# Optimization experiments

Hardware: AMD Instinct MI355X
Metric: run time of the kernel (lower is better)

## Reference

```python
import jax, jax.numpy as jnp
import numpy as np

NUM_EMBEDDINGS = 8192
EMBEDDING_DIM = 128


def setup_inputs() -> dict:
    key = jax.random.key(0)
    k1, k2 = jax.random.split(key)
    inputs = jax.random.normal(k1, (8, 32, 32, EMBEDDING_DIM), dtype=jnp.float32)
    embedding_weight = jax.random.normal(k2, (NUM_EMBEDDINGS, EMBEDDING_DIM), dtype=jnp.float32)
    return {"inputs": inputs, "embedding_weight": embedding_weight}


def reference(inputs, embedding_weight):
    # inputs: [B, H, W, C] channels-last; embedding_weight: [K, C]
    input_shape = inputs.shape
    flat_input = inputs.reshape(-1, EMBEDDING_DIM)  # [N, C]

    distances = (
        jnp.sum(flat_input ** 2, axis=1, keepdims=True)
        + jnp.sum(embedding_weight ** 2, axis=1)
        - 2.0 * flat_input @ embedding_weight.T
    )
    encoding_indices = jnp.argmin(distances, axis=1)  # [N]

    # one-hot encodings (returned by the original module)
    encodings = jax.nn.one_hot(encoding_indices, NUM_EMBEDDINGS, dtype=jnp.float32)  # [N, K]

    # quantized via direct gather (same math as one_hot @ weight, no big matmul)
    quantized = embedding_weight[encoding_indices].reshape(input_shape)  # [B,H,W,C]

    # straight-through estimator
    quantized = inputs + jax.lax.stop_gradient(quantized - inputs)

    quantized_nchw = jnp.transpose(quantized, (0, 3, 1, 2))  # [B,C,H,W]
    return quantized_nchw, encodings
```

## Files before the change

### kernel.cpp

```cpp
#include <hip/hip_runtime.h>

typedef _Float16 f16x4 __attribute__((ext_vector_type(4)));
typedef _Float16 f16x8 __attribute__((ext_vector_type(8)));
typedef float    f32x16 __attribute__((ext_vector_type(16)));
typedef float    f32x4v __attribute__((ext_vector_type(4)));

#define HN_OFF   0u
#define BEST_OFF 32768u
#define ERH_OFF  98304u
#define ERL_OFF  (98304u + 2097152u)
#define XRH_OFF  (98304u + 2u * 2097152u)
#define XRL_OFF  (98304u + 3u * 2097152u)

#define OUT_Q    0
#define OUT_ENC  1048576


__device__ __forceinline__ void gll16(const void* g, void* l) {
    __builtin_amdgcn_global_load_lds(
        (const __attribute__((address_space(1))) unsigned int*)g,
        (__attribute__((address_space(3))) unsigned int*)l, 16, 0, 0);
}

__global__ __launch_bounds__(256) void k1_convert(const float* __restrict__ x,
                                                  const float* __restrict__ e,
                                                  char* __restrict__ wsb) {
    int bx = blockIdx.x, tid = threadIdx.x;
    bool is_e = bx < 1024;
    const float* src = is_e ? e : x;
    int sec = is_e ? bx : bx - 1024;
    size_t off = (size_t)sec * 1024 + tid * 4;
    float4 v = *(const float4*)(src + off);

    f16x4 hi, lo;
    hi[0] = (_Float16)v.x; hi[1] = (_Float16)v.y;
    hi[2] = (_Float16)v.z; hi[3] = (_Float16)v.w;
    lo[0] = (_Float16)((v.x - (float)hi[0]) * 2048.0f);
    lo[1] = (_Float16)((v.y - (float)hi[1]) * 2048.0f);
    lo[2] = (_Float16)((v.z - (float)hi[2]) * 2048.0f);
    lo[3] = (_Float16)((v.w - (float)hi[3]) * 2048.0f);

    if (is_e) {
        int code = (int)(off >> 7);
        int c = (tid & 31) * 4;
        int tile = code >> 6, w = code & 63;
        int slot = (c >> 3) ^ (w & 15);
        size_t dst = (size_t)tile * 8192 + w * 128 + slot * 8 + (c & 7);
        *(f16x4*)((_Float16*)(wsb + ERH_OFF) + dst) = hi;
        *(f16x4*)((_Float16*)(wsb + ERL_OFF) + dst) = lo;

        float s = v.x * v.x + v.y * v.y + v.z * v.z + v.w * v.w;
        for (int o = 16; o > 0; o >>= 1) s += __shfl_down(s, o, 32);
        if ((tid & 31) == 0)
            ((float*)(wsb + HN_OFF))[code] = 0.5f * s;
    } else {
        _Float16* ph = (_Float16*)(wsb + XRH_OFF);
        _Float16* pl = (_Float16*)(wsb + XRL_OFF);
        *(f16x4*)(ph + off) = hi;
        *(f16x4*)(pl + off) = lo;
        if (sec < 32)
            ((unsigned long long*)(wsb + BEST_OFF))[sec * 256 + tid] = 0ull;
    }
}

__global__ __launch_bounds__(256, 2) void k2_mfma(char* __restrict__ wsb,
                                                  float* __restrict__ out) {
    __shared__ _Float16 lds_e[2][2][8192];
    __shared__ float    lds_hn[1024];

    const _Float16* xrh = (const _Float16*)(wsb + XRH_OFF);
    const _Float16* xrl = (const _Float16*)(wsb + XRL_OFF);
    const float* hn = (const float*)(wsb + HN_OFF);
    unsigned long long* bestg = (unsigned long long*)(wsb + BEST_OFF);

    int tid = threadIdx.x;
    int lane = tid & 63, wave = tid >> 6;
    int col = lane & 31, half = lane >> 5;
    int m = blockIdx.x;
    int by = m & 7, bx = m >> 3;
    int r0 = bx * 128;
    int k0g = by * 1024;
    int row = r0 + wave * 32 + col;

    f16x8 ah[8], al[8];
    #pragma unroll
    for (int s = 0; s < 8; s++) {
        ah[s] = *(const f16x8*)(xrh + (size_t)row * 128 + s * 16 + half * 8);
        al[s] = *(const f16x8*)(xrl + (size_t)row * 128 + s * 16 + half * 8);
    }

    *(float4*)(lds_hn + tid * 4) = *(const float4*)(hn + k0g + tid * 4);

    int plane = wave >> 1;
    int i0 = (wave & 1) * 8;
    const char* pbase = (const char*)wsb + (plane ? ERL_OFF : ERH_OFF);

    {
        const char* pb = pbase + (size_t)k0g * 256;
        #pragma unroll
        for (int j = 0; j < 8; j++) {
            int idx = i0 + j;
            gll16(pb + idx * 1024 + lane * 16,
                  (char*)&lds_e[0][plane][0] + idx * 1024);
        }
    }
    __syncthreads();

    float best[16];
    int bidx[16];
    #pragma unroll
    for (int i = 0; i < 16; i++) { best[i] = -3.0e38f; bidx[i] = 0; }

    float* encf = out + OUT_ENC;
    long zb4 = (long)(by * 64 + bx) * 32768;
    f32x4v z4 = {0.f, 0.f, 0.f, 0.f};

    int b = 0;
    for (int t = 0; t < 16; t++) {
        if (t < 15) {
            const char* pb = pbase + (size_t)(k0g + (t + 1) * 64) * 256;
            #pragma unroll
            for (int j = 0; j < 8; j++) {
                int idx = i0 + j;
                gll16(pb + idx * 1024 + lane * 16,
                      (char*)&lds_e[b ^ 1][plane][0] + idx * 1024);
            }
        }
        asm volatile("" ::: "memory");
        #pragma unroll
        for (int i = 0; i < 8; i++)
            __builtin_nontemporal_store(
                z4, (f32x4v*)encf + zb4 + t * 2048 + i * 256 + tid);

        #pragma unroll
        for (int sub = 0; sub < 2; sub++) {
            f32x16 a0, a1, a2;
            #pragma unroll
            for (int i = 0; i < 16; i++) { a0[i] = 0.f; a1[i] = 0.f; a2[i] = 0.f; }
            int cb = (sub * 32 + col) * 128;
            #pragma unroll
            for (int s = 0; s < 8; s++) {
                int so = ((s * 2 + half) ^ (col & 15)) * 8;
                f16x8 bh = *(const f16x8*)(&lds_e[b][0][cb + so]);
                f16x8 bl = *(const f16x8*)(&lds_e[b][1][cb + so]);
                a0 = __builtin_amdgcn_mfma_f32_32x32x16_f16(ah[s], bh, a0, 0, 0, 0);
                a1 = __builtin_amdgcn_mfma_f32_32x32x16_f16(ah[s], bl, a1, 0, 0, 0);
                a2 = __builtin_amdgcn_mfma_f32_32x32x16_f16(al[s], bh, a2, 0, 0, 0);
            }
            int code = k0g + t * 64 + sub * 32 + col;
            float hnv = lds_hn[t * 64 + sub * 32 + col];
            #pragma unroll
            for (int r = 0; r < 16; r++) {
                float sc = a0[r] + (a1[r] + a2[r]) * (1.0f / 2048.0f) - hnv;
                if (sc > best[r]) { best[r] = sc; bidx[r] = code; }
            }
        }

        asm volatile("s_waitcnt vmcnt(8)" ::: "memory");
        __builtin_amdgcn_s_barrier();
        b ^= 1;
    }

    #pragma unroll
    for (int r = 0; r < 16; r++) {
        float s = best[r];
        int bi = bidx[r];
        #pragma unroll
        for (int mm = 1; mm < 32; mm <<= 1) {
            float qs = __shfl_xor(s, mm, 64);
            int qi = __shfl_xor(bi, mm, 64);
            if (qs > s || (qs == s && qi < bi)) { s = qs; bi = qi; }
        }
        if (col == 0) {
            int rl = (r & 3) + 8 * (r >> 2) + 4 * half;
            unsigned ub = __float_as_uint(s);
            ub = ((int)ub < 0) ? ~ub : (ub | 0x80000000u);
            unsigned long long p = ((unsigned long long)ub << 32) |
                                   (unsigned long long)(0xFFFFFFFFu - (unsigned)bi);
            atomicMax(&bestg[r0 + wave * 32 + rl], p);
        }
    }
}

__global__ __launch_bounds__(256) void k3_final(const char* __restrict__ wsb,
                                                const float* __restrict__ wgt,
                                                float* __restrict__ out) {
    int bid = blockIdx.x;
    int n = (bid & 31) * 256 + threadIdx.x;
    int q = bid >> 5;
    unsigned long long p = ((const unsigned long long*)(wsb + BEST_OFF))[n];
    int bi = (int)(0xFFFFFFFFu - (unsigned)(p & 0xFFFFFFFFull));

    if (q == 0)
        out[(size_t)OUT_ENC + (size_t)n * 8192 + bi] = 1.0f;

    int bq = n >> 10, hw = n & 1023;
    float* o = out + (size_t)bq * 131072 + hw + (size_t)q * 32 * 1024;
    const float4* wrow = (const float4*)(wgt + (size_t)bi * 128) + q * 8;
    #pragma unroll
    for (int c4 = 0; c4 < 8; c4++) {
        float4 v = wrow[c4];
        o[(c4 * 4 + 0) * 1024] = v.x;
        o[(c4 * 4 + 1) * 1024] = v.y;
        o[(c4 * 4 + 2) * 1024] = v.z;
        o[(c4 * 4 + 3) * 1024] = v.w;
    }
}

extern "C" void kernel_launch(void* const* d_in, const int* in_sizes, int n_in,
                              void* d_out, int out_size, void* d_ws, size_t ws_size,
                              hipStream_t stream) {
    const float* x = (const float*)d_in[0];
    const float* e = (const float*)d_in[1];
    float* out = (float*)d_out;
    char* ws = (char*)d_ws;

    k1_convert<<<2048, 256, 0, stream>>>(x, e, ws);
    k2_mfma<<<512, 256, 0, stream>>>(ws, out);
    k3_final<<<128, 256, 0, stream>>>(ws, e, out);
}
```

Before: 297.3 us.

## Load codebook fragments directly from global memory instead of LDS staging

The codebook hi/lo planes are re-laid out so each lane's MFMA B fragment is a contiguous 16-byte global load. The LDS double buffer, global_load_lds prefetch and per-tile barriers are removed. The zero-fill of the encodings matrix changes from nontemporal stores to plain stores spread across the sub-tiles. This drops barrier synchronisation and LDS traffic, but B operands now come straight from L2/global with no software prefetch, so latency may be exposed, and each wave reloads the same codebook data.

After: 329.5 us. 10.9% more time.

```diff
diff --git a/kernel.cpp b/kernel.cpp
--- a/kernel.cpp
+++ b/kernel.cpp
@@ -15,12 +15,6 @@
 #define OUT_Q    0
 #define OUT_ENC  1048576
 
-
-__device__ __forceinline__ void gll16(const void* g, void* l) {
-    __builtin_amdgcn_global_load_lds(
-        (const __attribute__((address_space(1))) unsigned int*)g,
-        (__attribute__((address_space(3))) unsigned int*)l, 16, 0, 0);
-}
 
 __global__ __launch_bounds__(256) void k1_convert(const float* __restrict__ x,
                                                   const float* __restrict__ e,
@@ -44,15 +38,15 @@
         int code = (int)(off >> 7);
         int c = (tid & 31) * 4;
         int tile = code >> 6, w = code & 63;
-        int slot = (c >> 3) ^ (w & 15);
-        size_t dst = (size_t)tile * 8192 + w * 128 + slot * 8 + (c & 7);
+        int s = c >> 4, half = (c >> 3) & 1;
+        size_t dst = (size_t)tile * 8192 + s * 1024 + w * 16 + half * 8 + (c & 7);
         *(f16x4*)((_Float16*)(wsb + ERH_OFF) + dst) = hi;
         *(f16x4*)((_Float16*)(wsb + ERL_OFF) + dst) = lo;
 
-        float s = v.x * v.x + v.y * v.y + v.z * v.z + v.w * v.w;
-        for (int o = 16; o > 0; o >>= 1) s += __shfl_down(s, o, 32);
+        float ss = v.x * v.x + v.y * v.y + v.z * v.z + v.w * v.w;
+        for (int o = 16; o > 0; o >>= 1) ss += __shfl_down(ss, o, 32);
         if ((tid & 31) == 0)
-            ((float*)(wsb + HN_OFF))[code] = 0.5f * s;
+            ((float*)(wsb + HN_OFF))[code] = 0.5f * ss;
     } else {
         _Float16* ph = (_Float16*)(wsb + XRH_OFF);
         _Float16* pl = (_Float16*)(wsb + XRL_OFF);
@@ -65,11 +59,10 @@
 
 __global__ __launch_bounds__(256, 2) void k2_mfma(char* __restrict__ wsb,
                                                   float* __restrict__ out) {
-    __shared__ _Float16 lds_e[2][2][8192];
-    __shared__ float    lds_hn[1024];
-
     const _Float16* xrh = (const _Float16*)(wsb + XRH_OFF);
     const _Float16* xrl = (const _Float16*)(wsb + XRL_OFF);
+    const _Float16* erh = (const _Float16*)(wsb + ERH_OFF);
+    const _Float16* erl = (const _Float16*)(wsb + ERL_OFF);
     const float* hn = (const float*)(wsb + HN_OFF);
     unsigned long long* bestg = (unsigned long long*)(wsb + BEST_OFF);
 
@@ -89,76 +82,48 @@
         al[s] = *(const f16x8*)(xrl + (size_t)row * 128 + s * 16 + half * 8);
     }
 
-    *(float4*)(lds_hn + tid * 4) = *(const float4*)(hn + k0g + tid * 4);
-
-    int plane = wave >> 1;
-    int i0 = (wave & 1) * 8;
-    const char* pbase = (const char*)wsb + (plane ? ERL_OFF : ERH_OFF);
-
-    {
-        const char* pb = pbase + (size_t)k0g * 256;
-        #pragma unroll
-        for (int j = 0; j < 8; j++) {
-            int idx = i0 + j;
-            gll16(pb + idx * 1024 + lane * 16,
-                  (char*)&lds_e[0][plane][0] + idx * 1024);
-        }
-    }
-    __syncthreads();
+    int lane_eo = col * 16 + half * 8;
+    const _Float16* phz = erh + (size_t)(k0g >> 6) * 8192;
+    const _Float16* plz = erl + (size_t)(k0g >> 6) * 8192;
 
     float best[16];
     int bidx[16];
     #pragma unroll
     for (int i = 0; i < 16; i++) { best[i] = -3.0e38f; bidx[i] = 0; }
 
-    float* encf = out + OUT_ENC;
-    long zb4 = (long)(by * 64 + bx) * 32768;
     f32x4v z4 = {0.f, 0.f, 0.f, 0.f};
+    f32x4v* dstf = (f32x4v*)(out + OUT_ENC) + (size_t)(by * 64 + bx) * 32768 + tid;
 
-    int b = 0;
     for (int t = 0; t < 16; t++) {
-        if (t < 15) {
-            const char* pb = pbase + (size_t)(k0g + (t + 1) * 64) * 256;
-            #pragma unroll
-            for (int j = 0; j < 8; j++) {
-                int idx = i0 + j;
-                gll16(pb + idx * 1024 + lane * 16,
-                      (char*)&lds_e[b ^ 1][plane][0] + idx * 1024);
-            }
-        }
-        asm volatile("" ::: "memory");
-        #pragma unroll
-        for (int i = 0; i < 8; i++)
-            __builtin_nontemporal_store(
-                z4, (f32x4v*)encf + zb4 + t * 2048 + i * 256 + tid);
-
+        const _Float16* ph = phz + (size_t)t * 8192;
+        const _Float16* pl = plz + (size_t)t * 8192;
         #pragma unroll
         for (int sub = 0; sub < 2; sub++) {
             f32x16 a0, a1, a2;
             #pragma unroll
             for (int i = 0; i < 16; i++) { a0[i] = 0.f; a1[i] = 0.f; a2[i] = 0.f; }
-            int cb = (sub * 32 + col) * 128;
+            const _Float16* phs = ph + sub * 512 + lane_eo;
+            const _Float16* pls = pl + sub * 512 + lane_eo;
             #pragma unroll
             for (int s = 0; s < 8; s++) {
-                int so = ((s * 2 + half) ^ (col & 15)) * 8;
-                f16x8 bh = *(const f16x8*)(&lds_e[b][0][cb + so]);
-                f16x8 bl = *(const f16x8*)(&lds_e[b][1][cb + so]);
+                f16x8 bh = *(const f16x8*)(phs + s * 1024);
+                f16x8 bl = *(const f16x8*)(pls + s * 1024);
                 a0 = __builtin_amdgcn_mfma_f32_32x32x16_f16(ah[s], bh, a0, 0, 0, 0);
                 a1 = __builtin_amdgcn_mfma_f32_32x32x16_f16(ah[s], bl, a1, 0, 0, 0);
                 a2 = __builtin_amdgcn_mfma_f32_32x32x16_f16(al[s], bh, a2, 0, 0, 0);
             }
+            #pragma unroll
+            for (int i = 0; i < 4; i++)
+                dstf[(t * 2 + sub) * 1024 + i * 256] = z4;
+
             int code = k0g + t * 64 + sub * 32 + col;
-            float hnv = lds_hn[t * 64 + sub * 32 + col];
+            float hnv = hn[code];
             #pragma unroll
             for (int r = 0; r < 16; r++) {
                 float sc = a0[r] + (a1[r] + a2[r]) * (1.0f / 2048.0f) - hnv;
                 if (sc > best[r]) { best[r] = sc; bidx[r] = code; }
             }
         }
-
-        asm volatile("s_waitcnt vmcnt(8)" ::: "memory");
-        __builtin_amdgcn_s_barrier();
-        b ^= 1;
     }
 
     #pragma unroll
```
